# Kernel optimization log

Measured on AMD Instinct MI355X. Metric: run time of the kernel, lower is better.

## Reference

```python
import jax, jax.numpy as jnp
import numpy as np
from jax import lax

DN = ('NCHW', 'OIHW', 'NCHW')
BN_EPS = 1e-5

def conv2d(x, w, b=None, pad=0):
    y = lax.conv_general_dilated(x, w, (1, 1), [(pad, pad), (pad, pad)], dimension_numbers=DN)
    if b is not None:
        y = y + b[None, :, None, None]
    return y

def setup_inputs() -> dict:
    key = jax.random.key(0)
    ks = jax.random.split(key, 12)
    B, C, H, W = 8, 256, 64, 64
    ca = C // 4  # dim_att = 64
    s = 0.05  # weight scale to keep attention logits sane
    return {
        'x': jax.random.normal(ks[0], (B, C, H, W), jnp.float32),
        'w_dw1': jax.random.normal(ks[1], (ca // 2, ca, 7, 7), jnp.float32) * s,
        'b_dw1': jax.random.normal(ks[2], (ca // 2,), jnp.float32) * s,
        'w_dw2': jax.random.normal(ks[3], (ca // 2, ca, 11, 11), jnp.float32) * s,
        'b_dw2': jax.random.normal(ks[4], (ca // 2,), jnp.float32) * s,
        'w_k': jax.random.normal(ks[5], (ca, ca, 1, 1), jnp.float32) * s,
        'b_k': jax.random.normal(ks[6], (ca,), jnp.float32) * s,
        'w_v': jax.random.normal(ks[7], (ca, ca, 1, 1), jnp.float32) * s,
        'b_v': jax.random.normal(ks[8], (ca,), jnp.float32) * s,
        'w_c1': jax.random.normal(ks[9], (C, C, 1, 1), jnp.float32) * s,
        'bn_g': jnp.ones((C,), jnp.float32),
        'bn_b': jnp.zeros((C,), jnp.float32),
        'bn_m': jnp.zeros((C,), jnp.float32),
        'bn_var': jnp.ones((C,), jnp.float32),
        'w_c2': jax.random.normal(ks[10], (C, C, 1, 1), jnp.float32) * s,
        'b_c2': jax.random.normal(ks[11], (C,), jnp.float32) * s,
    }

def reference(x, w_dw1, b_dw1, w_dw2, b_dw2, w_k, b_k, w_v, b_v,
              w_c1, bn_g, bn_b, bn_m, bn_var, w_c2, b_c2):
    ca = w_k.shape[0]  # dim_att
    B, C, H, W = x.shape
    HW = H * W
    x1 = x[:, :ca]
    x2 = x[:, ca:]
    # Q from two multi-scale convs (7x7 and 11x11, same padding)
    q = jnp.concatenate([conv2d(x1, w_dw1, b_dw1, pad=3),
                         conv2d(x1, w_dw2, b_dw2, pad=5)], axis=1)  # [B,ca,H,W]
    q = q.reshape(B, ca, HW)                                         # [B,ca,HW]
    k = conv2d(x1, w_k, b_k).reshape(B, ca, HW)                      # [B,ca,HW]
    v = conv2d(x1, w_v, b_v).reshape(B, ca, HW)                      # [B,ca,HW]
    # att[b,n,m] = softmax_m( sum_c q[b,c,n] * k[b,c,m] )
    att = jax.nn.softmax(jnp.einsum('bcn,bcm->bnm', q, k), axis=-1)  # [B,HW,HW]
    # out1[b,c,n] = sum_m v[b,c,m] * att[b,n,m]
    out1 = jnp.einsum('bcm,bnm->bcn', v, att).reshape(B, ca, H, W)
    y = jnp.concatenate([out1, x2], axis=1)  # [B,C,H,W]
    # conv1 = YOLO Conv: 1x1 conv (no bias) + BatchNorm (eval stats) + SiLU
    y = conv2d(y, w_c1)
    inv = lax.rsqrt(bn_var + BN_EPS)
    y = (y - bn_m[None, :, None, None]) * (bn_g * inv)[None, :, None, None] + bn_b[None, :, None, None]
    y = jax.nn.silu(y)
    # conv2 = plain 1x1 conv with bias
    return conv2d(y, w_c2, b_c2)
```

## Files before the change

kernel.cpp:

```cpp
#include <hip/hip_runtime.h>

typedef __attribute__((ext_vector_type(8))) short frag8;
typedef __attribute__((ext_vector_type(4))) float f32x4;
typedef __attribute__((ext_vector_type(8))) unsigned short us8;
typedef __attribute__((ext_vector_type(4))) unsigned short us4;
typedef __attribute__((ext_vector_type(2))) unsigned int u32x2;

#define MFMA(a,b,c) __builtin_amdgcn_mfma_f32_16x16x32_bf16((a),(b),(c),0,0,0)

__device__ __forceinline__ unsigned short f2bf(float f){
  unsigned int u = __builtin_bit_cast(unsigned int, f);
  u += 0x7fffu + ((u >> 16) & 1u);
  return (unsigned short)(u >> 16);
}

__device__ __forceinline__ float bf2f(unsigned short h){
  unsigned int u = ((unsigned int)h) << 16;
  return __builtin_bit_cast(float, u);
}

__device__ __forceinline__ unsigned int cvt_pk_bf16(float a, float b){
  unsigned int r;
  asm volatile("v_cvt_pk_bf16_f32 %0, %1, %2" : "=v"(r) : "v"(a), "v"(b));
  return r;
}

#define OFF_XT   ((size_t)0)
#define OFF_KT   ((size_t)16777216)
#define OFF_VCT  ((size_t)20971520)
#define OFF_QT   ((size_t)25165824)
#define OFF_O1T  ((size_t)29360128)
#define OFF_ZT   ((size_t)33554432)
#define OFF_WQ7  ((size_t)50331648)
#define OFF_WQ11 ((size_t)50532352)
#define OFF_WC1  ((size_t)51027968)
#define OFF_WC2  ((size_t)51159040)
#define OFF_BC1  ((size_t)51290112)
#define OFF_WKB  ((size_t)51291136)
#define OFF_WVB  ((size_t)51299328)
#define OFF_ML2  OFF_WQ7
#define OFF_ML4  ((size_t)51307520)
#define WS_NEED4 ((size_t)(OFF_ML4 + 1048576))

__global__ __launch_bounds__(256) void prep_weights_kernel(
    const float* __restrict__ wdw1, const float* __restrict__ wdw2,
    const float* __restrict__ wc1, const float* __restrict__ bng,
    const float* __restrict__ bnb, const float* __restrict__ bnm,
    const float* __restrict__ bnv, const float* __restrict__ wc2,
    const float* __restrict__ wk, const float* __restrict__ wv,
    unsigned short* __restrict__ wq7, unsigned short* __restrict__ wq11,
    unsigned short* __restrict__ wc1b, unsigned short* __restrict__ wc2b,
    float* __restrict__ bc1, unsigned short* __restrict__ wkb,
    unsigned short* __restrict__ wvb){
  int i = blockIdx.x*256 + threadIdx.x;
  if (i < 100352){
    int o = i >> 11, rem = i & 2047;
    int co = rem >> 6, ci = rem & 63;
    int kh = o / 7, kw = o % 7;
    wq7[i] = f2bf(wdw1[(co*64 + ci)*49 + kh*7 + kw]);
  } else if (i < 348160){
    int j = i - 100352;
    int o = j >> 11, rem = j & 2047;
    int co = rem >> 6, ci = rem & 63;
    int kh = o / 11, kw = o % 11;
    wq11[j] = f2bf(wdw2[(co*64 + ci)*121 + kh*11 + kw]);
  } else if (i < 413696){
    int j = i - 348160;
    int co = j >> 8;
    float a = bng[co] * rsqrtf(bnv[co] + 1e-5f);
    wc1b[j] = f2bf(wc1[j] * a);
    if ((j & 255) == 0) bc1[co] = bnb[co] - bnm[co]*a;
  } else if (i < 479232){
    int j = i - 413696;
    wc2b[j] = f2bf(wc2[j]);
  } else if (i < 483328){
    int j = i - 479232;
    wkb[j] = f2bf(wk[j]);
  } else if (i < 487424){
    int j = i - 483328;
    wvb[j] = f2bf(wv[j]);
  }
}

__global__ __launch_bounds__(256) void prep_x_kernel(const float* __restrict__ x,
                                                     unsigned short* __restrict__ xt){
  int g = blockIdx.x*256 + threadIdx.x;
  int b = g >> 12, n = g & 4095;
  int c0base = blockIdx.y * 64;
  const float* xp = x + (((size_t)b*256) << 12) + n;
  unsigned short* op = xt + (size_t)g*256;
  for (int c0 = c0base; c0 < c0base + 64; c0 += 8){
    us8 v;
    #pragma unroll
    for (int j = 0; j < 8; ++j) v[j] = f2bf(xp[(size_t)(c0+j) << 12]);
    *reinterpret_cast<us8*>(op + c0) = v;
  }
}

__global__ __launch_bounds__(256) void kv_kernel(const unsigned short* __restrict__ xt,
    const unsigned short* __restrict__ wkb, const unsigned short* __restrict__ wvb,
    const float* __restrict__ bk, const float* __restrict__ bv,
    unsigned short* __restrict__ kt, unsigned short* __restrict__ vct){
  int gid = blockIdx.x;
  int part = gid >> 9, t = gid & 511;
  int b = t >> 6, tile = t & 63;
  int lane = threadIdx.x & 63, wid = threadIdx.x >> 6;
  int lo = lane & 15, hi = lane >> 4;
  int n0 = tile*64 + wid*16;
  size_t bb = (size_t)b << 12;
  f32x4 acc[4];
  #pragma unroll
  for (int f = 0; f < 4; ++f) acc[f] = (f32x4){0.f,0.f,0.f,0.f};
  frag8 x0 = *reinterpret_cast<const frag8*>(xt + (bb + n0 + lo)*256 + 8*hi);
  frag8 x1 = *reinterpret_cast<const frag8*>(xt + (bb + n0 + lo)*256 + 32 + 8*hi);
  if (part == 0){
    #pragma unroll
    for (int nf = 0; nf < 4; ++nf){
      frag8 w0 = *reinterpret_cast<const frag8*>(wkb + (nf*16 + lo)*64 + 8*hi);
      frag8 w1 = *reinterpret_cast<const frag8*>(wkb + (nf*16 + lo)*64 + 32 + 8*hi);
      acc[nf] = MFMA(x0, w0, acc[nf]);
      acc[nf] = MFMA(x1, w1, acc[nf]);
    }
    #pragma unroll
    for (int nf = 0; nf < 4; ++nf){
      int co = nf*16 + lo;
      float bias = bk[co];
      #pragma unroll
      for (int r = 0; r < 4; ++r)
        kt[(bb + n0 + hi*4 + r)*64 + co] = f2bf(acc[nf][r] + bias);
    }
  } else {
    #pragma unroll
    for (int mf = 0; mf < 4; ++mf){
      frag8 w0 = *reinterpret_cast<const frag8*>(wvb + (mf*16 + lo)*64 + 8*hi);
      frag8 w1 = *reinterpret_cast<const frag8*>(wvb + (mf*16 + lo)*64 + 32 + 8*hi);
      acc[mf] = MFMA(w0, x0, acc[mf]);
      acc[mf] = MFMA(w1, x1, acc[mf]);
    }
    #pragma unroll
    for (int mf = 0; mf < 4; ++mf){
      #pragma unroll
      for (int r = 0; r < 4; ++r){
        int c = mf*16 + hi*4 + r;
        vct[(((size_t)b*64 + c) << 12) + n0 + lo] = f2bf(acc[mf][r] + bv[c]);
      }
    }
  }
}

template<int KS>
__global__ __launch_bounds__(256) void conv_q_kernel(const unsigned short* __restrict__ xt,
    const unsigned short* __restrict__ wq, const float* __restrict__ bias,
    unsigned short* __restrict__ qt){
  constexpr int P = KS/2;
  constexpr int NR = (KS+1)/2;
  __shared__ unsigned short xs[NR*64*64];
  __shared__ float outst[2][64][33];
  int h0 = blockIdx.x*2, b = blockIdx.y;
  int tid = threadIdx.x, lane = tid & 63, wid = tid >> 6;
  int lo = lane & 15, hi = lane >> 4;
  int cofrag = wid & 1, hsel = wid >> 1;
  int h = h0 + hsel;
  f32x4 acc[4];
  #pragma unroll
  for (int nf = 0; nf < 4; ++nf) acc[nf] = (f32x4){0.f,0.f,0.f,0.f};
  const size_t xbase = ((size_t)b << 12) * 256;
  #pragma unroll
  for (int pass = 0; pass < 2; ++pass){
    const int srcBase = h0 - P + pass*NR;
    if (pass) __syncthreads();
    for (int idx = tid; idx < NR*512; idx += 256){
      int rl = idx >> 9, w = (idx >> 3) & 63, ch = idx & 7;
      int sr = srcBase + rl;
      us8 v = {0,0,0,0,0,0,0,0};
      if (sr >= 0 && sr < 64)
        v = *reinterpret_cast<const us8*>(xt + xbase + (size_t)(sr*64 + w)*256 + ch*8);
      int byte = (rl*64 + w)*128 + ((ch*16) ^ ((w & 7) << 4));
      *reinterpret_cast<us8*>((char*)xs + byte) = v;
    }
    __syncthreads();
    for (int rl = 0; rl < NR; ++rl){
      int dh = srcBase + rl - h + P;
      if (dh < 0 || dh >= KS) continue;
      frag8 wf[KS][2];
      int off0 = dh*KS;
      #pragma unroll
      for (int dw = 0; dw < KS; ++dw){
        #pragma unroll
        for (int ks = 0; ks < 2; ++ks)
          wf[dw][ks] = *reinterpret_cast<const frag8*>(
              wq + (size_t)(off0+dw)*2048 + (cofrag*16 + lo)*64 + ks*32 + 8*hi);
      }
      #pragma unroll
      for (int dw = 0; dw < KS; ++dw){
        #pragma unroll
        for (int nf = 0; nf < 4; ++nf){
          int w_out = nf*16 + lo;
          int wp = w_out + dw - P;
          frag8 bx0 = {0,0,0,0,0,0,0,0}, bx1 = {0,0,0,0,0,0,0,0};
          if (wp >= 0 && wp < 64){
            int rowb = (rl*64 + wp)*128;
            int sw = (wp & 7) << 4;
            bx0 = *reinterpret_cast<const frag8*>((char*)xs + rowb + ((hi*16) ^ sw));
            bx1 = *reinterpret_cast<const frag8*>((char*)xs + rowb + ((64 + hi*16) ^ sw));
          }
          acc[nf] = MFMA(wf[dw][0], bx0, acc[nf]);
          acc[nf] = MFMA(wf[dw][1], bx1, acc[nf]);
        }
      }
    }
  }
  #pragma unroll
  for (int nf = 0; nf < 4; ++nf){
    int w = nf*16 + lo;
    #pragma unroll
    for (int r = 0; r < 4; ++r)
      outst[hsel][w][cofrag*16 + hi*4 + r] = acc[nf][r];
  }
  __syncthreads();
  {
    int hs = tid >> 7, rem = tid & 127;
    int w = rem >> 1, c16 = (rem & 1)*16;
    int cobase = (KS == 7) ? 0 : 32;
    size_t qrow = (((size_t)b << 12) + (h0 + hs)*64 + w)*64;
    #pragma unroll
    for (int g = 0; g < 2; ++g){
      int c8 = c16 + g*8;
      us8 v;
      #pragma unroll
      for (int j = 0; j < 8; ++j) v[j] = f2bf(outst[hs][w][c8 + j] + bias[c8 + j]);
      *reinterpret_cast<us8*>(qt + qrow + cobase + c8) = v;
    }
  }
}

template<int NSPLIT>
__global__ __launch_bounds__(256, 2) void attn_kernel(const unsigned short* __restrict__ qt,
    const unsigned short* __restrict__ kt, const unsigned short* __restrict__ vct,
    unsigned short* __restrict__ opart, float* __restrict__ mlpart){
  constexpr int TILES = 64 / NSPLIT;
  __shared__ unsigned short kls[2][64*64];
  __shared__ unsigned short vls[2][64*64];
  __shared__ unsigned short pls[4][32*64];
  int b = blockIdx.y, half = blockIdx.z;
  int tid = threadIdx.x, lane = tid & 63, wid = tid >> 6;
  int lo = lane & 15, hi = lane >> 4;
  int q0 = blockIdx.x*128 + wid*32;
  const size_t bb = (size_t)b << 12;
  const int mtbase = half * TILES;
  const int sm = tid >> 3, sch = tid & 7;
  const int dstA = sm*128 + ((sch*16) ^ ((sm & 7) << 4));
  const int dstB = dstA + 32*128;
  char* pbase = (char*)pls[wid];
  frag8 aq[2][2];
  #pragma unroll
  for (int mf = 0; mf < 2; ++mf)
    #pragma unroll
    for (int ks = 0; ks < 2; ++ks)
      aq[mf][ks] = *reinterpret_cast<const frag8*>(
          qt + (bb + q0 + mf*16 + lo)*64 + ks*32 + 8*hi);
  f32x4 o[2][4];
  #pragma unroll
  for (int mf = 0; mf < 2; ++mf)
    #pragma unroll
    for (int f = 0; f < 4; ++f) o[mf][f] = (f32x4){0.f,0.f,0.f,0.f};
  float mr[2]  = {-1e30f, -1e30f};
  float lr[2]  = {0.f, 0.f};
  float mrT[2][4];
  #pragma unroll
  for (int mf = 0; mf < 2; ++mf)
    #pragma unroll
    for (int r = 0; r < 4; ++r) mrT[mf][r] = -1e30f;
  us8 kr0, kr1, vr0, vr1;
  {
    int mt = mtbase;
    kr0 = *reinterpret_cast<const us8*>(kt + (bb + mt*64 + sm)*64 + sch*8);
    kr1 = *reinterpret_cast<const us8*>(kt + (bb + mt*64 + sm + 32)*64 + sch*8);
    vr0 = *reinterpret_cast<const us8*>(vct + (((size_t)b*64 + sm) << 12) + mt*64 + sch*8);
    vr1 = *reinterpret_cast<const us8*>(vct + (((size_t)b*64 + sm + 32) << 12) + mt*64 + sch*8);
    *reinterpret_cast<us8*>((char*)kls[0] + dstA) = kr0;
    *reinterpret_cast<us8*>((char*)kls[0] + dstB) = kr1;
    *reinterpret_cast<us8*>((char*)vls[0] + dstA) = vr0;
    *reinterpret_cast<us8*>((char*)vls[0] + dstB) = vr1;
  }
  __syncthreads();
  int cur = 0;
  for (int t = 0; t < TILES; ++t){
    if (t < TILES-1){
      int mt = mtbase + t + 1;
      kr0 = *reinterpret_cast<const us8*>(kt + (bb + mt*64 + sm)*64 + sch*8);
      kr1 = *reinterpret_cast<const us8*>(kt + (bb + mt*64 + sm + 32)*64 + sch*8);
      vr0 = *reinterpret_cast<const us8*>(vct + (((size_t)b*64 + sm) << 12) + mt*64 + sch*8);
      vr1 = *reinterpret_cast<const us8*>(vct + (((size_t)b*64 + sm + 32) << 12) + mt*64 + sch*8);
    }
    f32x4 s[2][4];
    #pragma unroll
    for (int mf = 0; mf < 2; ++mf)
      #pragma unroll
      for (int f = 0; f < 4; ++f) s[mf][f] = (f32x4){0.f,0.f,0.f,0.f};
    #pragma unroll
    for (int nf = 0; nf < 4; ++nf){
      int m = nf*16 + lo;
      int sw = (m & 7) << 4;
      frag8 b0 = *reinterpret_cast<const frag8*>((char*)kls[cur] + m*128 + ((hi*16) ^ sw));
      frag8 b1 = *reinterpret_cast<const frag8*>((char*)kls[cur] + m*128 + ((64 + hi*16) ^ sw));
      s[0][nf] = MFMA(b0, aq[0][0], s[0][nf]);
      s[0][nf] = MFMA(b1, aq[0][1], s[0][nf]);
      s[1][nf] = MFMA(b0, aq[1][0], s[1][nf]);
      s[1][nf] = MFMA(b1, aq[1][1], s[1][nf]);
    }
    float pm[2];
    #pragma unroll
    for (int mf = 0; mf < 2; ++mf){
      float a0 = fmaxf(fmaxf(s[mf][0][0], s[mf][0][1]), fmaxf(s[mf][0][2], s[mf][0][3]));
      float a1 = fmaxf(fmaxf(s[mf][1][0], s[mf][1][1]), fmaxf(s[mf][1][2], s[mf][1][3]));
      float a2 = fmaxf(fmaxf(s[mf][2][0], s[mf][2][1]), fmaxf(s[mf][2][2], s[mf][2][3]));
      float a3 = fmaxf(fmaxf(s[mf][3][0], s[mf][3][1]), fmaxf(s[mf][3][2], s[mf][3][3]));
      pm[mf] = fmaxf(fmaxf(a0, a1), fmaxf(a2, a3));
    }
    float growth = fmaxf(pm[0] - mr[0], pm[1] - mr[1]);
    if (!__all(growth <= 8.0f)){
      float rmax[2] = {pm[0], pm[1]};
      #pragma unroll
      for (int mf = 0; mf < 2; ++mf){
        rmax[mf] = fmaxf(rmax[mf], __shfl_xor(rmax[mf], 16));
        rmax[mf] = fmaxf(rmax[mf], __shfl_xor(rmax[mf], 32));
        float mn = fmaxf(mr[mf], rmax[mf]);
        lr[mf] *= __expf(mr[mf] - mn);
        mr[mf] = mn;
      }
      #pragma unroll
      for (int mf = 0; mf < 2; ++mf)
        #pragma unroll
        for (int r = 0; r < 4; ++r){
          float mnT = __shfl(mr[mf], hi*4 + r);
          float scT = __expf(mrT[mf][r] - mnT);
          mrT[mf][r] = mnT;
          #pragma unroll
          for (int nf = 0; nf < 4; ++nf) o[mf][nf][r] *= scT;
        }
    }
    #pragma unroll
    for (int mf = 0; mf < 2; ++mf){
      float acc = 0.f;
      #pragma unroll
      for (int nf = 0; nf < 4; ++nf){
        #pragma unroll
        for (int r = 0; r < 4; ++r){
          s[mf][nf][r] = __expf(s[mf][nf][r] - mr[mf]);
          acc += s[mf][nf][r];
        }
        u32x2 w;
        w[0] = cvt_pk_bf16(s[mf][nf][0], s[mf][nf][1]);
        w[1] = cvt_pk_bf16(s[mf][nf][2], s[mf][nf][3]);
        *reinterpret_cast<u32x2*>(pbase + (mf*16 + lo)*128 +
            ((nf*32 + hi*8) ^ ((lo & 7) << 4))) = w;
      }
      lr[mf] += acc;
    }
    #pragma unroll
    for (int ks = 0; ks < 2; ++ks){
      frag8 ap0 = *reinterpret_cast<const frag8*>(
          pbase + lo*128 + ((ks*64 + hi*16) ^ ((lo & 7) << 4)));
      frag8 ap1 = *reinterpret_cast<const frag8*>(
          pbase + (16 + lo)*128 + ((ks*64 + hi*16) ^ ((lo & 7) << 4)));
      #pragma unroll
      for (int nf = 0; nf < 4; ++nf){
        int c = nf*16 + lo;
        frag8 bv = *reinterpret_cast<const frag8*>(
            (char*)vls[cur] + c*128 + ((ks*64 + hi*16) ^ ((c & 7) << 4)));
        o[0][nf] = MFMA(ap0, bv, o[0][nf]);
        o[1][nf] = MFMA(ap1, bv, o[1][nf]);
      }
    }
    if (t < TILES-1){
      *reinterpret_cast<us8*>((char*)kls[cur^1] + dstA) = kr0;
      *reinterpret_cast<us8*>((char*)kls[cur^1] + dstB) = kr1;
      *reinterpret_cast<us8*>((char*)vls[cur^1] + dstA) = vr0;
      *reinterpret_cast<us8*>((char*)vls[cur^1] + dstB) = vr1;
    }
    __syncthreads();
    cur ^= 1;
  }
  #pragma unroll
  for (int mf = 0; mf < 2; ++mf){
    lr[mf] += __shfl_xor(lr[mf], 16);
    lr[mf] += __shfl_xor(lr[mf], 32);
  }
  size_t pb = ((size_t)(half*8 + b) << 12);
  #pragma unroll
  for (int mf = 0; mf < 2; ++mf){
    #pragma unroll
    for (int nf = 0; nf < 4; ++nf)
      #pragma unroll
      for (int r = 0; r < 4; ++r)
        opart[(pb + q0 + mf*16 + hi*4 + r)*64 + nf*16 + lo] = f2bf(o[mf][nf][r]);
    if (hi == 0){
      size_t idx = pb + q0 + mf*16 + lo;
      mlpart[idx*2]     = mr[mf];
      mlpart[idx*2 + 1] = lr[mf];
    }
  }
}

template<int NSPLIT>
__global__ __launch_bounds__(256) void merge_kernel(const unsigned short* __restrict__ opart,
    const float* __restrict__ mlpart, unsigned short* __restrict__ o1t){
  int g = blockIdx.x*256 + threadIdx.x;
  int c4 = g & 15, q = (g >> 4) & 4095, b = g >> 16;
  size_t idx[NSPLIT];
  float m[NSPLIT], l[NSPLIT];
  float M = -1e30f;
  #pragma unroll
  for (int p = 0; p < NSPLIT; ++p){
    idx[p] = ((size_t)(p*8 + b) << 12) + q;
    m[p] = mlpart[idx[p]*2];
    l[p] = mlpart[idx[p]*2 + 1];
    M = fmaxf(M, m[p]);
  }
  float denom = 0.f, w[NSPLIT];
  #pragma unroll
  for (int p = 0; p < NSPLIT; ++p){
    w[p] = __expf(m[p] - M);
    denom += w[p] * l[p];
  }
  float inv = 1.0f / denom;
  f32x4 acc = (f32x4){0.f,0.f,0.f,0.f};
  #pragma unroll
  for (int p = 0; p < NSPLIT; ++p){
    us4 a = *reinterpret_cast<const us4*>(opart + idx[p]*64 + c4*4);
    float wp = w[p] * inv;
    #pragma unroll
    for (int j = 0; j < 4; ++j) acc[j] += wp * bf2f(a[j]);
  }
  unsigned short outv[4];
  #pragma unroll
  for (int j = 0; j < 4; ++j) outv[j] = f2bf(acc[j]);
  *reinterpret_cast<ulonglong1*>(o1t + (((size_t)b << 12) + q)*64 + c4*4) =
      *reinterpret_cast<ulonglong1*>(outv);
}

__global__ __launch_bounds__(256) void c1_kernel(const unsigned short* __restrict__ o1t,
    const unsigned short* __restrict__ xt, const unsigned short* __restrict__ wc1b,
    const float* __restrict__ bc1, unsigned short* __restrict__ zt){
  int b = blockIdx.y;
  int q0 = blockIdx.x*64 + (threadIdx.x >> 6)*16;
  int lane = threadIdx.x & 63, lo = lane & 15, hi = lane >> 4;
  size_t bb = (size_t)b << 12;
  f32x4 acc[16];
  #pragma unroll
  for (int nf = 0; nf < 16; ++nf) acc[nf] = (f32x4){0.f,0.f,0.f,0.f};
  #pragma unroll
  for (int ks = 0; ks < 8; ++ks){
    int ci0 = ks*32 + 8*hi;
    frag8 a;
    if (ks < 2) a = *reinterpret_cast<const frag8*>(o1t + (bb + q0 + lo)*64 + ci0);
    else        a = *reinterpret_cast<const frag8*>(xt  + (bb + q0 + lo)*256 + ci0);
    #pragma unroll
    for (int nf = 0; nf < 16; ++nf){
      frag8 w = *reinterpret_cast<const frag8*>(wc1b + (nf*16 + lo)*256 + ci0);
      acc[nf] = MFMA(a, w, acc[nf]);
    }
  }
  #pragma unroll
  for (int nf = 0; nf < 16; ++nf){
    int co = nf*16 + lo;
    float bias = bc1[co];
    #pragma unroll
    for (int r = 0; r < 4; ++r){
      float y = acc[nf][r] + bias;
      y = y / (1.0f + __expf(-y));
      zt[(bb + q0 + hi*4 + r)*256 + co] = f2bf(y);
    }
  }
}

__global__ __launch_bounds__(256) void c2_kernel(const unsigned short* __restrict__ zt,
    const unsigned short* __restrict__ wc2b, const float* __restrict__ bc2,
    float* __restrict__ out){
  int b = blockIdx.y;
  int q0 = blockIdx.x*128 + (threadIdx.x >> 6)*32;
  int lane = threadIdx.x & 63, lo = lane & 15, hi = lane >> 4;
  size_t bb = (size_t)b << 12;
  f32x4 acc[16][2];
  #pragma unroll
  for (int mf = 0; mf < 16; ++mf){
    acc[mf][0] = (f32x4){0.f,0.f,0.f,0.f};
    acc[mf][1] = (f32x4){0.f,0.f,0.f,0.f};
  }
  #pragma unroll
  for (int ks = 0; ks < 8; ++ks){
    int ci0 = ks*32 + 8*hi;
    frag8 bz0 = *reinterpret_cast<const frag8*>(zt + (bb + q0 + lo)*256 + ci0);
    frag8 bz1 = *reinterpret_cast<const frag8*>(zt + (bb + q0 + 16 + lo)*256 + ci0);
    #pragma unroll
    for (int mf = 0; mf < 16; ++mf){
      frag8 aw = *reinterpret_cast<const frag8*>(wc2b + (mf*16 + lo)*256 + ci0);
      acc[mf][0] = MFMA(aw, bz0, acc[mf][0]);
      acc[mf][1] = MFMA(aw, bz1, acc[mf][1]);
    }
  }
  #pragma unroll
  for (int mf = 0; mf < 16; ++mf){
    #pragma unroll
    for (int r = 0; r < 4; ++r){
      int co = mf*16 + hi*4 + r;
      float bias = bc2[co];
      float* op = out + (((size_t)b*256 + co) << 12) + q0 + lo;
      op[0]  = acc[mf][0][r] + bias;
      op[16] = acc[mf][1][r] + bias;
    }
  }
}

extern "C" void kernel_launch(void* const* d_in, const int* in_sizes, int n_in,
                              void* d_out, int out_size, void* d_ws, size_t ws_size,
                              hipStream_t stream){
  const float* x    = (const float*)d_in[0];
  const float* wdw1 = (const float*)d_in[1];
  const float* bdw1 = (const float*)d_in[2];
  const float* wdw2 = (const float*)d_in[3];
  const float* bdw2 = (const float*)d_in[4];
  const float* wk   = (const float*)d_in[5];
  const float* bk   = (const float*)d_in[6];
  const float* wv   = (const float*)d_in[7];
  const float* bv   = (const float*)d_in[8];
  const float* wc1  = (const float*)d_in[9];
  const float* bng  = (const float*)d_in[10];
  const float* bnb  = (const float*)d_in[11];
  const float* bnm  = (const float*)d_in[12];
  const float* bnv  = (const float*)d_in[13];
  const float* wc2  = (const float*)d_in[14];
  const float* bc2  = (const float*)d_in[15];
  char* ws = (char*)d_ws;
  unsigned short* xt   = (unsigned short*)(ws + OFF_XT);
  unsigned short* ktp  = (unsigned short*)(ws + OFF_KT);
  unsigned short* vct  = (unsigned short*)(ws + OFF_VCT);
  unsigned short* qtp  = (unsigned short*)(ws + OFF_QT);
  unsigned short* o1t  = (unsigned short*)(ws + OFF_O1T);
  unsigned short* zt   = (unsigned short*)(ws + OFF_ZT);
  unsigned short* wq7  = (unsigned short*)(ws + OFF_WQ7);
  unsigned short* wq11 = (unsigned short*)(ws + OFF_WQ11);
  unsigned short* wc1b = (unsigned short*)(ws + OFF_WC1);
  unsigned short* wc2b = (unsigned short*)(ws + OFF_WC2);
  float*          bc1  = (float*)(ws + OFF_BC1);
  unsigned short* wkb  = (unsigned short*)(ws + OFF_WKB);
  unsigned short* wvb  = (unsigned short*)(ws + OFF_WVB);
  unsigned short* opart = (unsigned short*)(ws + OFF_ZT);
  const bool big = (ws_size >= WS_NEED4);
  float*          mlp   = (float*)(ws + (big ? OFF_ML4 : OFF_ML2));

  prep_weights_kernel<<<1904, 256, 0, stream>>>(wdw1, wdw2, wc1, bng, bnb, bnm, bnv,
                                                wc2, wk, wv, wq7, wq11, wc1b, wc2b,
                                                bc1, wkb, wvb);
  prep_x_kernel<<<dim3(128, 4), 256, 0, stream>>>(x, xt);
  kv_kernel<<<1024, 256, 0, stream>>>(xt, wkb, wvb, bk, bv, ktp, vct);
  conv_q_kernel<7><<<dim3(32, 8), 256, 0, stream>>>(xt, wq7, bdw1, qtp);
  conv_q_kernel<11><<<dim3(32, 8), 256, 0, stream>>>(xt, wq11, bdw2, qtp);
  if (big){
    attn_kernel<4><<<dim3(32, 8, 4), 256, 0, stream>>>(qtp, ktp, vct, opart, mlp);
    merge_kernel<4><<<2048, 256, 0, stream>>>(opart, mlp, o1t);
  } else {
    attn_kernel<2><<<dim3(32, 8, 2), 256, 0, stream>>>(qtp, ktp, vct, opart, mlp);
    merge_kernel<2><<<2048, 256, 0, stream>>>(opart, mlp, o1t);
  }
  c1_kernel<<<dim3(64, 8), 256, 0, stream>>>(o1t, xt, wc1b, bc1, zt);
  c2_kernel<<<dim3(32, 8), 256, 0, stream>>>(zt, wc2b, bc2, (float*)d_out);
}
```

Before: 233.2 us.

## Load V fragments directly from global memory and fold log2e into Q

The attention kernel no longer stages V tiles through LDS. Each wave loads its V MFMA operand fragments straight from global memory every tile, which removes the LDS writes and reads for V and halves the kernel's LDS footprint. Q is pre-scaled by log2(e) when it is written, so the softmax uses exp2f directly, and the rescale threshold and merge kernel are adjusted to match. The cost is redundant global/L2 traffic for V across the four waves, plus load latency that is no longer prefetched a tile ahead.

```diff
diff --git a/kernel.cpp b/kernel.cpp
--- a/kernel.cpp
+++ b/kernel.cpp
@@ -7,6 +7,7 @@
 typedef __attribute__((ext_vector_type(2))) unsigned int u32x2;
 
 #define MFMA(a,b,c) __builtin_amdgcn_mfma_f32_16x16x32_bf16((a),(b),(c),0,0,0)
+#define LOG2E 1.44269504f
 
 __device__ __forceinline__ unsigned short f2bf(float f){
   unsigned int u = __builtin_bit_cast(unsigned int, f);
@@ -228,7 +229,8 @@
       int c8 = c16 + g*8;
       us8 v;
       #pragma unroll
-      for (int j = 0; j < 8; ++j) v[j] = f2bf(outst[hs][w][c8 + j] + bias[c8 + j]);
+      for (int j = 0; j < 8; ++j)
+        v[j] = f2bf((outst[hs][w][c8 + j] + bias[c8 + j]) * LOG2E);
       *reinterpret_cast<us8*>(qt + qrow + cobase + c8) = v;
     }
   }
@@ -240,7 +242,6 @@
     unsigned short* __restrict__ opart, float* __restrict__ mlpart){
   constexpr int TILES = 64 / NSPLIT;
   __shared__ unsigned short kls[2][64*64];
-  __shared__ unsigned short vls[2][64*64];
   __shared__ unsigned short pls[4][32*64];
   int b = blockIdx.y, half = blockIdx.z;
   int tid = threadIdx.x, lane = tid & 63, wid = tid >> 6;
@@ -252,6 +253,7 @@
   const int dstA = sm*128 + ((sch*16) ^ ((sm & 7) << 4));
   const int dstB = dstA + 32*128;
   char* pbase = (char*)pls[wid];
+  const unsigned short* vb = vct + (((size_t)b*64) << 12);
   frag8 aq[2][2];
   #pragma unroll
   for (int mf = 0; mf < 2; ++mf)
@@ -271,27 +273,29 @@
   for (int mf = 0; mf < 2; ++mf)
     #pragma unroll
     for (int r = 0; r < 4; ++r) mrT[mf][r] = -1e30f;
-  us8 kr0, kr1, vr0, vr1;
+  us8 kr0, kr1;
   {
     int mt = mtbase;
     kr0 = *reinterpret_cast<const us8*>(kt + (bb + mt*64 + sm)*64 + sch*8);
     kr1 = *reinterpret_cast<const us8*>(kt + (bb + mt*64 + sm + 32)*64 + sch*8);
-    vr0 = *reinterpret_cast<const us8*>(vct + (((size_t)b*64 + sm) << 12) + mt*64 + sch*8);
-    vr1 = *reinterpret_cast<const us8*>(vct + (((size_t)b*64 + sm + 32) << 12) + mt*64 + sch*8);
     *reinterpret_cast<us8*>((char*)kls[0] + dstA) = kr0;
     *reinterpret_cast<us8*>((char*)kls[0] + dstB) = kr1;
-    *reinterpret_cast<us8*>((char*)vls[0] + dstA) = vr0;
-    *reinterpret_cast<us8*>((char*)vls[0] + dstB) = vr1;
   }
   __syncthreads();
   int cur = 0;
   for (int t = 0; t < TILES; ++t){
+    int mt = mtbase + t;
+    frag8 bvr[2][4];
+    #pragma unroll
+    for (int ks = 0; ks < 2; ++ks)
+      #pragma unroll
+      for (int cf = 0; cf < 4; ++cf)
+        bvr[ks][cf] = *reinterpret_cast<const frag8*>(
+            vb + (((size_t)(cf*16 + lo)) << 12) + mt*64 + ks*32 + hi*8);
     if (t < TILES-1){
-      int mt = mtbase + t + 1;
-      kr0 = *reinterpret_cast<const us8*>(kt + (bb + mt*64 + sm)*64 + sch*8);
-      kr1 = *reinterpret_cast<const us8*>(kt + (bb + mt*64 + sm + 32)*64 + sch*8);
-      vr0 = *reinterpret_cast<const us8*>(vct + (((size_t)b*64 + sm) << 12) + mt*64 + sch*8);
-      vr1 = *reinterpret_cast<const us8*>(vct + (((size_t)b*64 + sm + 32) << 12) + mt*64 + sch*8);
+      int mtn = mt + 1;
+      kr0 = *reinterpret_cast<const us8*>(kt + (bb + mtn*64 + sm)*64 + sch*8);
+      kr1 = *reinterpret_cast<const us8*>(kt + (bb + mtn*64 + sm + 32)*64 + sch*8);
     }
     f32x4 s[2][4];
     #pragma unroll
@@ -319,14 +323,14 @@
       pm[mf] = fmaxf(fmaxf(a0, a1), fmaxf(a2, a3));
     }
     float growth = fmaxf(pm[0] - mr[0], pm[1] - mr[1]);
-    if (!__all(growth <= 8.0f)){
+    if (!__all(growth <= 11.5416f)){
       float rmax[2] = {pm[0], pm[1]};
       #pragma unroll
       for (int mf = 0; mf < 2; ++mf){
         rmax[mf] = fmaxf(rmax[mf], __shfl_xor(rmax[mf], 16));
         rmax[mf] = fmaxf(rmax[mf], __shfl_xor(rmax[mf], 32));
         float mn = fmaxf(mr[mf], rmax[mf]);
-        lr[mf] *= __expf(mr[mf] - mn);
+        lr[mf] *= exp2f(mr[mf] - mn);
         mr[mf] = mn;
       }
       #pragma unroll
@@ -334,10 +338,10 @@
         #pragma unroll
         for (int r = 0; r < 4; ++r){
           float mnT = __shfl(mr[mf], hi*4 + r);
-          float scT = __expf(mrT[mf][r] - mnT);
+          float scT = exp2f(mrT[mf][r] - mnT);
           mrT[mf][r] = mnT;
           #pragma unroll
-          for (int nf = 0; nf < 4; ++nf) o[mf][nf][r] *= scT;
+          for (int cf = 0; cf < 4; ++cf) o[mf][cf][r] *= scT;
         }
     }
     #pragma unroll
@@ -347,7 +351,7 @@
       for (int nf = 0; nf < 4; ++nf){
         #pragma unroll
         for (int r = 0; r < 4; ++r){
-          s[mf][nf][r] = __expf(s[mf][nf][r] - mr[mf]);
+          s[mf][nf][r] = exp2f(s[mf][nf][r] - mr[mf]);
           acc += s[mf][nf][r];
         }
         u32x2 w;
@@ -365,19 +369,14 @@
       frag8 ap1 = *reinterpret_cast<const frag8*>(
           pbase + (16 + lo)*128 + ((ks*64 + hi*16) ^ ((lo & 7) << 4)));
       #pragma unroll
-      for (int nf = 0; nf < 4; ++nf){
-        int c = nf*16 + lo;
-        frag8 bv = *reinterpret_cast<const frag8*>(
-            (char*)vls[cur] + c*128 + ((ks*64 + hi*16) ^ ((c & 7) << 4)));
-        o[0][nf] = MFMA(ap0, bv, o[0][nf]);
-        o[1][nf] = MFMA(ap1, bv, o[1][nf]);
+      for (int cf = 0; cf < 4; ++cf){
+        o[0][cf] = MFMA(ap0, bvr[ks][cf], o[0][cf]);
+        o[1][cf] = MFMA(ap1, bvr[ks][cf], o[1][cf]);
       }
     }
     if (t < TILES-1){
       *reinterpret_cast<us8*>((char*)kls[cur^1] + dstA) = kr0;
       *reinterpret_cast<us8*>((char*)kls[cur^1] + dstB) = kr1;
-      *reinterpret_cast<us8*>((char*)vls[cur^1] + dstA) = vr0;
-      *reinterpret_cast<us8*>((char*)vls[cur^1] + dstB) = vr1;
     }
     __syncthreads();
     cur ^= 1;
@@ -391,10 +390,10 @@
   #pragma unroll
   for (int mf = 0; mf < 2; ++mf){
     #pragma unroll
-    for (int nf = 0; nf < 4; ++nf)
+    for (int cf = 0; cf < 4; ++cf)
       #pragma unroll
       for (int r = 0; r < 4; ++r)
-        opart[(pb + q0 + mf*16 + hi*4 + r)*64 + nf*16 + lo] = f2bf(o[mf][nf][r]);
+        opart[(pb + q0 + mf*16 + hi*4 + r)*64 + cf*16 + lo] = f2bf(o[mf][cf][r]);
     if (hi == 0){
       size_t idx = pb + q0 + mf*16 + lo;
       mlpart[idx*2]     = mr[mf];
@@ -421,7 +420,7 @@
   float denom = 0.f, w[NSPLIT];
   #pragma unroll
   for (int p = 0; p < NSPLIT; ++p){
-    w[p] = __expf(m[p] - M);
+    w[p] = exp2f(m[p] - M);
     denom += w[p] * l[p];
   }
   float inv = 1.0f / denom;
```

After: 261.9 us. 1.12x slower.
